# Optimization experiments

Measured on AMD Instinct MI355X. Metric: run time of the kernel, lower is better.

## Reference

```python
import jax, jax.numpy as jnp
import numpy as np

N = 3000          # num_sample (nodes)
N_OMICS = 3000    # input feature dims for both omics
ENC1, ENC2, NZ = 256, 128, 64


def _xavier(key, fan_in, fan_out):
    limit = float(np.sqrt(6.0 / (fan_in + fan_out)))
    return jax.random.uniform(key, (fan_in, fan_out), jnp.float32, -limit, limit)


def setup_inputs() -> dict:
    key = jax.random.key(0)
    ks = jax.random.split(key, 20)
    inp = {
        "omics_1": jax.random.normal(ks[0], (N, N_OMICS), jnp.float32),
        "omics_2": jax.random.normal(ks[1], (N, N_OMICS), jnp.float32),
    }
    # random dense adjacency, row-normalized (as a typical normalized graph operator)
    for i, name in enumerate(["adj_feature_omics1", "adj_feature_omics2",
                              "adj_spatial_omics1", "adj_spatial_omics2"]):
        a = jax.random.uniform(ks[2 + i], (N, N), jnp.float32)
        inp[name] = a / jnp.sum(a, axis=1, keepdims=True)
    # GNNLayer weights for the four GAE encoders (xavier uniform, as in reset_parameters)
    dims = [(N_OMICS, ENC1), (ENC1, ENC2), (ENC2, NZ)]
    kidx = 6
    for enc in ["f1", "f2", "s1", "s2"]:
        for li, (fi, fo) in enumerate(dims, start=1):
            inp[f"w_{enc}_{li}"] = _xavier(ks[kidx], fi, fo)
            kidx += 1
    return inp


def _gae_encoder(x, adj, w1, w2, w3):
    # GNNLayer: support = act(x @ W); out = spmm(adj, support). Dropout is identity (eval).
    z = adj @ jnp.tanh(x @ w1)          # [N, ENC1]
    z = adj @ jnp.tanh(z @ w2)          # [N, ENC2]
    z = adj @ (z @ w3)                  # [N, NZ]  (no activation on layer 3)
    adj_hat = jax.nn.sigmoid(z @ z.T)   # [N, N]
    return z, adj_hat


def reference(omics_1, omics_2,
              adj_feature_omics1, adj_feature_omics2,
              adj_spatial_omics1, adj_spatial_omics2,
              w_f1_1, w_f1_2, w_f1_3,
              w_f2_1, w_f2_2, w_f2_3,
              w_s1_1, w_s1_2, w_s1_3,
              w_s2_1, w_s2_2, w_s2_3):
    _, a1 = _gae_encoder(omics_1, adj_feature_omics1, w_f1_1, w_f1_2, w_f1_3)
    _, a2 = _gae_encoder(omics_2, adj_feature_omics2, w_f2_1, w_f2_2, w_f2_3)
    _, a3 = _gae_encoder(omics_1, adj_spatial_omics1, w_s1_1, w_s1_2, w_s1_3)
    _, a4 = _gae_encoder(omics_2, adj_spatial_omics2, w_s2_1, w_s2_2, w_s2_3)
    # stacked reconstructed adjacencies from the four encoders [4, N, N]
    return jnp.stack([a1, a2, a3, a4], axis=0)
```

## Files before the change

### kernel.cpp

```cpp
#include <hip/hip_runtime.h>
#include <stdint.h>
#include <stddef.h>


typedef __attribute__((ext_vector_type(8))) _Float16 half8;
typedef __attribute__((ext_vector_type(4))) float f32x4;

#define PAD 3072
#define MR  3000
#define ADJ_STRIDE ((size_t)PAD * PAD)

static __device__ __forceinline__ void async_cp16(const _Float16* g, _Float16* l) {
    __builtin_amdgcn_global_load_lds((const __attribute__((address_space(1))) void*)g,
                                     (__attribute__((address_space(3))) void*)l, 16, 0, 0);
}

struct Wt12 { const float* src[12]; _Float16* dst[12];
              int fi[12]; int fo[12]; int ldk[12]; int nr[12]; };

__global__ __launch_bounds__(256) void wt_cast12(Wt12 p) {
    const int z   = blockIdx.y;
    const int idx = blockIdx.x * 256 + threadIdx.x;
    const int ldk = p.ldk[z];
    if (idx >= p.nr[z] * ldk) return;
    const int r = idx / ldk;
    const int k = idx - r * ldk;
    float v = 0.f;
    if (r < p.fo[z] && k < p.fi[z]) v = p.src[z][(size_t)k * p.fo[z] + r];
    p.dst[z][(size_t)r * ldk + k] = (_Float16)v;
}

struct GArgs {
    const _Float16* Aall; size_t aStride;
    const _Float16* Ball; size_t bStride;
    const float* Bf0; const float* Bf1;
    void* Call; size_t cStride;
    int M, Ncols, Kp, lda, ldb, ldc, mBound, nBound;
};

template<int ACT, int OMODE, int S, int BSRC>
static __device__ __forceinline__
void gemm_body(const GArgs& ga, int bx, int by, int bz, _Float16* smem)
{
    _Float16* As = smem;
    _Float16* Bs = smem + 8192;

    const int z   = bz;
    const int e   = z / S;
    const int ksl = z - e * S;
    const int Kslice = ga.Kp / S;
    const int kbase  = ksl * Kslice;

    const _Float16* A = ga.Aall + (size_t)e * ga.aStride;
    const _Float16* B = ga.Ball + (size_t)e * ga.bStride;
    const float*    Bf = (e & 1) ? ga.Bf1 : ga.Bf0;

    const int tm = bx * 128;
    const int tn = by * 128;
    const int t    = threadIdx.x;
    const int lane = t & 63;
    const int w    = t >> 6;
    const int wm   = (w >> 1) * 64;
    const int wn   = (w & 1) * 64;
    const int lr   = lane & 15;
    const int lg   = lane >> 4;

    f32x4 acc[4][4];
    const f32x4 zero = {0.f, 0.f, 0.f, 0.f};
    #pragma unroll
    for (int i = 0; i < 4; ++i)
        #pragma unroll
        for (int j = 0; j < 4; ++j) acc[i][j] = zero;

    const int nkt = Kslice >> 6;
    for (int kt = 0; kt < nkt; ++kt) {
        const int k0 = kbase + (kt << 6);
        #pragma unroll
        for (int i = 0; i < 4; ++i) {
            const int c = t + i * 256;
            const int row = c >> 3, slot = c & 7;
            const int ss = slot ^ (row & 7);
            async_cp16(A + (size_t)(tm + row) * ga.lda + k0 + ss * 8, &As[c * 8]);
        }
        if (BSRC) {
            #pragma unroll
            for (int i = 0; i < 4; ++i) {
                const int c = t + i * 256;
                const int row = c >> 3, g = c & 7;
                const int grow = tn + row;
                const int gcol = k0 + g * 8;
                half8 h;
                if (grow < MR && gcol < MR) {
                    const float* bp = Bf + (size_t)grow * MR + gcol;
                    f32x4 v0 = *(const f32x4*)bp;
                    f32x4 v1 = *(const f32x4*)(bp + 4);
                    #pragma unroll
                    for (int j = 0; j < 4; ++j) { h[j] = (_Float16)v0[j]; h[4 + j] = (_Float16)v1[j]; }
                } else {
                    #pragma unroll
                    for (int j = 0; j < 8; ++j) h[j] = (_Float16)0.f;
                }
                *(half8*)&Bs[row * 64 + ((g ^ (row & 7)) << 3)] = h;
            }
        } else {
            #pragma unroll
            for (int i = 0; i < 4; ++i) {
                const int c = t + i * 256;
                const int row = c >> 3, slot = c & 7;
                const int ss = slot ^ (row & 7);
                async_cp16(B + (size_t)(tn + row) * ga.ldb + k0 + ss * 8, &Bs[c * 8]);
            }
        }
        __syncthreads();

        #pragma unroll
        for (int ks = 0; ks < 2; ++ks) {
            half8 af[4], bf[4];
            #pragma unroll
            for (int mi = 0; mi < 4; ++mi) {
                const int ra = wm + mi * 16 + lr;
                const int s  = (ks * 4 + lg) ^ (ra & 7);
                af[mi] = *(const half8*)((const char*)As + ra * 128 + s * 16);
            }
            #pragma unroll
            for (int ni = 0; ni < 4; ++ni) {
                const int rb = wn + ni * 16 + lr;
                const int s  = (ks * 4 + lg) ^ (rb & 7);
                bf[ni] = *(const half8*)((const char*)Bs + rb * 128 + s * 16);
            }
            #pragma unroll
            for (int mi = 0; mi < 4; ++mi)
                #pragma unroll
                for (int ni = 0; ni < 4; ++ni)
                    acc[mi][ni] = __builtin_amdgcn_mfma_f32_16x16x32_f16(
                        af[mi], bf[ni], acc[mi][ni], 0, 0, 0);
        }
        __syncthreads();
    }

    if (OMODE == 0) {
        _Float16* C = (_Float16*)ga.Call + (size_t)e * ga.cStride;
        #pragma unroll
        for (int mi = 0; mi < 4; ++mi)
            #pragma unroll
            for (int rr = 0; rr < 4; ++rr) {
                const int m = tm + wm + mi * 16 + lg * 4 + rr;
                #pragma unroll
                for (int ni = 0; ni < 4; ++ni) {
                    const int n = tn + wn + ni * 16 + lr;
                    float x = acc[mi][ni][rr];
                    if (ACT) x = tanhf(x);
                    const bool ok = (m < ga.M) && (n < ga.Ncols);
                    C[(size_t)m * ga.ldc + n] = ok ? (_Float16)x : (_Float16)0.f;
                }
            }
    } else {
        float* Cp = (float*)ga.Call + (size_t)(OMODE == 3 ? z : e) * ga.cStride;
        float* ep = (float*)smem + w * 2048;
        #pragma unroll
        for (int hs = 0; hs < 2; ++hs) {
            __syncthreads();
            #pragma unroll
            for (int mi2 = 0; mi2 < 2; ++mi2)
                #pragma unroll
                for (int ni = 0; ni < 4; ++ni)
                    #pragma unroll
                    for (int rr = 0; rr < 4; ++rr) {
                        const int row = mi2 * 16 + lg * 4 + rr;
                        const int col = ni * 16 + lr;
                        const int sw  = (((row ^ (row >> 2)) & 3) << 4);
                        ep[row * 64 + (col ^ sw)] = acc[hs * 2 + mi2][ni][rr];
                    }
            __syncthreads();
            #pragma unroll
            for (int r2 = 0; r2 < 8; ++r2) {
                const int row = r2 * 4 + (lane >> 4);
                const int c4  = (lane & 15) * 4;
                const int sw  = (((row ^ (row >> 2)) & 3) << 4);
                f32x4 v = *(const f32x4*)&ep[row * 64 + (c4 ^ sw)];
                const int gm = tm + wm + hs * 32 + row;
                const int gn = tn + wn + c4;
                if (gm < ga.mBound && gn < ga.nBound) {
                    if (OMODE == 2) {
                        #pragma unroll
                        for (int j = 0; j < 4; ++j)
                            v[j] = 1.0f / (1.0f + __expf(-v[j]));
                    }
                    *(f32x4*)&Cp[(size_t)gm * ga.ldc + gn] = v;
                }
            }
        }
    }
}

template<int ACT, int OMODE, int S, int BSRC>
__global__ __launch_bounds__(256, 2)
void gemm_bt(GArgs ga) {
    __shared__ _Float16 smem[16384];
    gemm_body<ACT, OMODE, S, BSRC>(ga, blockIdx.x, blockIdx.y, blockIdx.z, smem);
}

struct Adj4 { const float* src[4]; };

__global__ __launch_bounds__(256, 2)
void fused_s1(GArgs ga, Adj4 a4, _Float16* __restrict__ adst)
{
    __shared__ _Float16 smem[16384];
    const int b = blockIdx.x;
    if (b < 768) {
        const int bz = b & 15;
        const int r  = b >> 4;
        gemm_body<0, 3, 4, 1>(ga, r & 1, r >> 1, bz, smem);
    } else {
        const int cb  = b - 768;
        const int zz  = cb / 2304;
        const int idx = (cb - zz * 2304) * 256 + threadIdx.x;
        const int row = idx / 192;
        const int u   = idx - row * 192;
        const int c0  = u * 16;
        const float* sp = a4.src[zz] + (size_t)row * MR + c0;
        _Float16* d = adst + (size_t)zz * ADJ_STRIDE + (size_t)row * PAD + c0;
        half8 h0, h1;
        const bool rok = row < MR;
        if (rok && c0 < MR) {
            f32x4 v0 = __builtin_nontemporal_load((const f32x4*)sp);
            f32x4 v1 = __builtin_nontemporal_load((const f32x4*)(sp + 4));
            #pragma unroll
            for (int j = 0; j < 4; ++j) { h0[j] = (_Float16)v0[j]; h0[4 + j] = (_Float16)v1[j]; }
        } else {
            #pragma unroll
            for (int j = 0; j < 8; ++j) h0[j] = (_Float16)0.f;
        }
        if (rok && c0 + 8 < MR) {
            f32x4 v2 = __builtin_nontemporal_load((const f32x4*)(sp + 8));
            f32x4 v3 = __builtin_nontemporal_load((const f32x4*)(sp + 12));
            #pragma unroll
            for (int j = 0; j < 4; ++j) { h1[j] = (_Float16)v2[j]; h1[4 + j] = (_Float16)v3[j]; }
        } else {
            #pragma unroll
            for (int j = 0; j < 8; ++j) h1[j] = (_Float16)0.f;
        }
        *(half8*)d = h0;
        *(half8*)(d + 8) = h1;
    }
}

template<int ACT, int S>
__global__ __launch_bounds__(256)
void reduce_k(const float* __restrict__ P, _Float16* __restrict__ out, size_t region)
{
    const size_t e    = blockIdx.y;
    const size_t base = (size_t)(blockIdx.x * 256 + threadIdx.x) * 8;
    const float* p0 = P + e * S * region + base;
    f32x4 s0 = {0.f, 0.f, 0.f, 0.f}, s1 = s0;
    #pragma unroll
    for (int s = 0; s < S; ++s) {
        const float* p = p0 + (size_t)s * region;
        s0 += *(const f32x4*)p;
        s1 += *(const f32x4*)(p + 4);
    }
    half8 h;
    #pragma unroll
    for (int j = 0; j < 8; ++j) {
        float x = (j < 4) ? s0[j] : s1[j - 4];
        if (ACT) x = tanhf(x);
        h[j] = (_Float16)x;
    }
    *(half8*)(out + e * region + base) = h;
}

extern "C" void kernel_launch(void* const* d_in, const int* in_sizes, int n_in,
                              void* d_out, int out_size, void* d_ws, size_t ws_size,
                              hipStream_t stream)
{
    const float* X1 = (const float*)d_in[0];
    const float* X2 = (const float*)d_in[1];

    const size_t R1 = 786432;
    const size_t R2 = 393216;

    _Float16* Adj  = (_Float16*)d_out;
    float*    Part = (float*)(Adj + 4 * ADJ_STRIDE);

    _Float16* hb = (_Float16*)d_ws;
    size_t off = 0;
    auto alloc = [&](size_t elems) { _Float16* p = hb + off; off += elems; return p; };
    _Float16* T1  = alloc(4 * R1);
    _Float16* Z1  = alloc(4 * R1);
    _Float16* T2  = alloc(4 * R2);
    _Float16* Z2  = alloc(4 * R2);
    _Float16* T3  = alloc(4 * R2);
    _Float16* Z3  = alloc(4 * R2);
    _Float16* W1t = alloc(4ull * 256 * PAD);
    _Float16* W2t = alloc(4ull * 128 * 256);
    _Float16* W3t = alloc(4ull * 128 * 128);

    Wt12 w12;
    for (int enc = 0; enc < 4; ++enc) {
        w12.src[enc]     = (const float*)d_in[6 + enc * 3 + 0];
        w12.dst[enc]     = W1t + (size_t)enc * 256 * PAD;
        w12.fi[enc] = MR;  w12.fo[enc] = 256; w12.ldk[enc] = PAD; w12.nr[enc] = 256;

        w12.src[4 + enc] = (const float*)d_in[6 + enc * 3 + 1];
        w12.dst[4 + enc] = W2t + (size_t)enc * 128 * 256;
        w12.fi[4 + enc] = 256; w12.fo[4 + enc] = 128; w12.ldk[4 + enc] = 256; w12.nr[4 + enc] = 128;

        w12.src[8 + enc] = (const float*)d_in[6 + enc * 3 + 2];
        w12.dst[8 + enc] = W3t + (size_t)enc * 128 * 128;
        w12.fi[8 + enc] = 128; w12.fo[8 + enc] = 64; w12.ldk[8 + enc] = 128; w12.nr[8 + enc] = 128;
    }
    wt_cast12<<<dim3(3072, 12, 1), 256, 0, stream>>>(w12);

    const int BIG = 1 << 30;

    GArgs g1 = { W1t, (size_t)256 * PAD, nullptr, 0, X1, X2,
                 Part, R1, 256, PAD, PAD, PAD, MR, PAD, BIG, BIG };
    Adj4 a4;
    for (int i = 0; i < 4; ++i) a4.src[i] = (const float*)d_in[2 + i];
    fused_s1<<<dim3(9984, 1, 1), 256, 0, stream>>>(g1, a4, Adj);
    reduce_k<1, 4><<<dim3(384, 4, 1), 256, 0, stream>>>(Part, T1, R1);

    GArgs g2 = { Adj, ADJ_STRIDE, T1, R1, nullptr, nullptr,
                 Part, R1, PAD, 256, PAD, PAD, PAD, 256, BIG, BIG };
    gemm_bt<0, 3, 4, 0><<<dim3(24, 2, 16), 256, 0, stream>>>(g2);
    reduce_k<0, 4><<<dim3(384, 4, 1), 256, 0, stream>>>(Part, Z1, R1);

    GArgs g3 = { W2t, (size_t)128 * 256, Z1, R1, nullptr, nullptr,
                 Part, R2, 128, PAD, 256, 256, 256, PAD, BIG, BIG };
    gemm_bt<0, 3, 2, 0><<<dim3(1, 24, 8), 256, 0, stream>>>(g3);
    reduce_k<1, 2><<<dim3(192, 4, 1), 256, 0, stream>>>(Part, T2, R2);

    GArgs g4 = { Adj, ADJ_STRIDE, T2, R2, nullptr, nullptr,
                 Part, R2, PAD, 128, PAD, PAD, PAD, 128, BIG, BIG };
    gemm_bt<0, 3, 8, 0><<<dim3(24, 1, 32), 256, 0, stream>>>(g4);
    reduce_k<0, 8><<<dim3(192, 4, 1), 256, 0, stream>>>(Part, Z2, R2);

    GArgs g5 = { W3t, (size_t)128 * 128, Z2, R2, nullptr, nullptr,
                 T3, R2, 128, PAD, 128, 128, 128, PAD, BIG, BIG };
    gemm_bt<0, 0, 1, 0><<<dim3(1, 24, 4), 256, 0, stream>>>(g5);

    GArgs g6 = { Adj, ADJ_STRIDE, T3, R2, nullptr, nullptr,
                 Part, R2, PAD, 128, PAD, PAD, PAD, 128, BIG, BIG };
    gemm_bt<0, 3, 8, 0><<<dim3(24, 1, 32), 256, 0, stream>>>(g6);
    reduce_k<0, 8><<<dim3(192, 4, 1), 256, 0, stream>>>(Part, Z3, R2);

    GArgs g7 = { Z3, R2, Z3, R2, nullptr, nullptr,
                 d_out, (size_t)MR * MR, MR, MR, 64, 128, 128, MR, MR, MR };
    gemm_bt<0, 2, 1, 0><<<dim3(24, 24, 4), 256, 0, stream>>>(g7);
}
```

Measured before the change: 274.4 us.

## Pre-cast omics to fp16 and drop split-K for feature-projection GEMMs

Measured after the change: 282.2 us. 1.03x slower.

```diff
diff --git a/kernel.cpp b/kernel.cpp
--- a/kernel.cpp
+++ b/kernel.cpp
@@ -15,30 +15,94 @@
                                      (__attribute__((address_space(3))) void*)l, 16, 0, 0);
 }
 
-struct Wt12 { const float* src[12]; _Float16* dst[12];
-              int fi[12]; int fo[12]; int ldk[12]; int nr[12]; };
-
-__global__ __launch_bounds__(256) void wt_cast12(Wt12 p) {
-    const int z   = blockIdx.y;
-    const int idx = blockIdx.x * 256 + threadIdx.x;
-    const int ldk = p.ldk[z];
-    if (idx >= p.nr[z] * ldk) return;
-    const int r = idx / ldk;
-    const int k = idx - r * ldk;
-    float v = 0.f;
-    if (r < p.fo[z] && k < p.fi[z]) v = p.src[z][(size_t)k * p.fo[z] + r];
-    p.dst[z][(size_t)r * ldk + k] = (_Float16)v;
+struct PrepArgs {
+    const float* X[2]; _Float16* Xh;
+    const float* Wsrc[12];
+    _Float16* Wdst[3];
+};
+
+__global__ __launch_bounds__(256) void prep(PrepArgs p) {
+    __shared__ _Float16 lt[64 * 64];
+    const int b = blockIdx.x;
+    const int t = threadIdx.x;
+    if (b < 4608) {
+        const int which = b / 2304;
+        const int idx = (b - which * 2304) * 256 + t;
+        const int row = idx / 192;
+        const int c0  = (idx - row * 192) * 16;
+        const float* sp = p.X[which] + (size_t)row * MR + c0;
+        _Float16* d = p.Xh + (size_t)which * ADJ_STRIDE + (size_t)row * PAD + c0;
+        half8 h0, h1;
+        const bool rok = row < MR;
+        if (rok && c0 < MR) {
+            f32x4 v0 = __builtin_nontemporal_load((const f32x4*)sp);
+            f32x4 v1 = __builtin_nontemporal_load((const f32x4*)(sp + 4));
+            #pragma unroll
+            for (int j = 0; j < 4; ++j) { h0[j] = (_Float16)v0[j]; h0[4 + j] = (_Float16)v1[j]; }
+        } else {
+            #pragma unroll
+            for (int j = 0; j < 8; ++j) h0[j] = (_Float16)0.f;
+        }
+        if (rok && c0 + 8 < MR) {
+            f32x4 v2 = __builtin_nontemporal_load((const f32x4*)(sp + 8));
+            f32x4 v3 = __builtin_nontemporal_load((const f32x4*)(sp + 12));
+            #pragma unroll
+            for (int j = 0; j < 4; ++j) { h1[j] = (_Float16)v2[j]; h1[4 + j] = (_Float16)v3[j]; }
+        } else {
+            #pragma unroll
+            for (int j = 0; j < 8; ++j) h1[j] = (_Float16)0.f;
+        }
+        *(half8*)d = h0;
+        *(half8*)(d + 8) = h1;
+    } else {
+        const int b2  = b - 4608;
+        const int enc = b2 / 204;
+        int rem = b2 - enc * 204;
+        const float* src; _Float16* dst; int fi, fo, ldk, kt, rt;
+        if (rem < 192) {
+            src = p.Wsrc[enc * 3 + 0]; dst = p.Wdst[0] + (size_t)enc * 256 * PAD;
+            fi = MR; fo = 256; ldk = PAD; kt = rem >> 2; rt = rem & 3;
+        } else if (rem < 200) {
+            rem -= 192;
+            src = p.Wsrc[enc * 3 + 1]; dst = p.Wdst[1] + (size_t)enc * 128 * 256;
+            fi = 256; fo = 128; ldk = 256; kt = rem >> 1; rt = rem & 1;
+        } else {
+            rem -= 200;
+            src = p.Wsrc[enc * 3 + 2]; dst = p.Wdst[2] + (size_t)enc * 128 * 128;
+            fi = 128; fo = 64; ldk = 128; kt = rem >> 1; rt = rem & 1;
+        }
+        const int k0 = kt * 64, r0 = rt * 64;
+        {
+            const int kr = t >> 2, cc = (t & 3) << 4;
+            const int gk = k0 + kr;
+            const bool kok = gk < fi;
+            #pragma unroll
+            for (int j = 0; j < 16; ++j) {
+                const int gr = r0 + cc + j;
+                const float v = (kok && gr < fo) ? src[(size_t)gk * fo + gr] : 0.f;
+                lt[(cc + j) * 64 + kr] = (_Float16)v;
+            }
+        }
+        __syncthreads();
+        {
+            const int rr = t >> 2, kk = (t & 3) << 4;
+            half8 a  = *(half8*)&lt[rr * 64 + kk];
+            half8 bb = *(half8*)&lt[rr * 64 + kk + 8];
+            _Float16* dp = dst + (size_t)(r0 + rr) * ldk + k0 + kk;
+            *(half8*)dp = a;
+            *(half8*)(dp + 8) = bb;
+        }
+    }
 }
 
 struct GArgs {
-    const _Float16* Aall; size_t aStride;
-    const _Float16* Ball; size_t bStride;
-    const float* Bf0; const float* Bf1;
+    const _Float16* Aall; size_t aStride; int aMask;
+    const _Float16* Ball; size_t bStride; int bMask;
     void* Call; size_t cStride;
     int M, Ncols, Kp, lda, ldb, ldc, mBound, nBound;
 };
 
-template<int ACT, int OMODE, int S, int BSRC>
+template<int ACT, int OMODE, int S>
 static __device__ __forceinline__
 void gemm_body(const GArgs& ga, int bx, int by, int bz, _Float16* smem)
 {
@@ -51,9 +115,8 @@
     const int Kslice = ga.Kp / S;
     const int kbase  = ksl * Kslice;
 
-    const _Float16* A = ga.Aall + (size_t)e * ga.aStride;
-    const _Float16* B = ga.Ball + (size_t)e * ga.bStride;
-    const float*    Bf = (e & 1) ? ga.Bf1 : ga.Bf0;
+    const _Float16* A = ga.Aall + (size_t)(e & ga.aMask) * ga.aStride;
+    const _Float16* B = ga.Ball + (size_t)(e & ga.bMask) * ga.bStride;
 
     const int tm = bx * 128;
     const int tn = by * 128;
@@ -82,34 +145,12 @@
             const int ss = slot ^ (row & 7);
             async_cp16(A + (size_t)(tm + row) * ga.lda + k0 + ss * 8, &As[c * 8]);
         }
-        if (BSRC) {
-            #pragma unroll
-            for (int i = 0; i < 4; ++i) {
-                const int c = t + i * 256;
-                const int row = c >> 3, g = c & 7;
-                const int grow = tn + row;
-                const int gcol = k0 + g * 8;
-                half8 h;
-                if (grow < MR && gcol < MR) {
-                    const float* bp = Bf + (size_t)grow * MR + gcol;
-                    f32x4 v0 = *(const f32x4*)bp;
-                    f32x4 v1 = *(const f32x4*)(bp + 4);
-                    #pragma unroll
-                    for (int j = 0; j < 4; ++j) { h[j] = (_Float16)v0[j]; h[4 + j] = (_Float16)v1[j]; }
-                } else {
-                    #pragma unroll
-                    for (int j = 0; j < 8; ++j) h[j] = (_Float16)0.f;
-                }
-                *(half8*)&Bs[row * 64 + ((g ^ (row & 7)) << 3)] = h;
-            }
-        } else {
-            #pragma unroll
-            for (int i = 0; i < 4; ++i) {
-                const int c = t + i * 256;
-                const int row = c >> 3, slot = c & 7;
-                const int ss = slot ^ (row & 7);
-                async_cp16(B + (size_t)(tn + row) * ga.ldb + k0 + ss * 8, &Bs[c * 8]);
-            }
+        #pragma unroll
+        for (int i = 0; i < 4; ++i) {
+            const int c = t + i * 256;
+            const int row = c >> 3, slot = c & 7;
+            const int ss = slot ^ (row & 7);
+            async_cp16(B + (size_t)(tn + row) * ga.ldb + k0 + ss * 8, &Bs[c * 8]);
         }
         __syncthreads();
 
@@ -193,11 +234,11 @@
     }
 }
 
-template<int ACT, int OMODE, int S, int BSRC>
+template<int ACT, int OMODE, int S>
 __global__ __launch_bounds__(256, 2)
 void gemm_bt(GArgs ga) {
     __shared__ _Float16 smem[16384];
-    gemm_body<ACT, OMODE, S, BSRC>(ga, blockIdx.x, blockIdx.y, blockIdx.z, smem);
+    gemm_body<ACT, OMODE, S>(ga, blockIdx.x, blockIdx.y, blockIdx.z, smem);
 }
 
 struct Adj4 { const float* src[4]; };
@@ -207,12 +248,12 @@
 {
     __shared__ _Float16 smem[16384];
     const int b = blockIdx.x;
-    if (b < 768) {
-        const int bz = b & 15;
-        const int r  = b >> 4;
-        gemm_body<0, 3, 4, 1>(ga, r & 1, r >> 1, bz, smem);
+    if (b < 192) {
+        const int e   = b / 48;
+        const int rem = b - e * 48;
+        gemm_body<1, 0, 1>(ga, rem & 1, rem >> 1, e, smem);
     } else {
-        const int cb  = b - 768;
+        const int cb  = b - 192;
         const int zz  = cb / 2304;
         const int idx = (cb - zz * 2304) * 256 + threadIdx.x;
         const int row = idx / 192;
@@ -245,7 +286,7 @@
     }
 }
 
-template<int ACT, int S>
+template<int S>
 __global__ __launch_bounds__(256)
 void reduce_k(const float* __restrict__ P, _Float16* __restrict__ out, size_t region)
 {
@@ -261,11 +302,8 @@
     }
     half8 h;
     #pragma unroll
-    for (int j = 0; j < 8; ++j) {
-        float x = (j < 4) ? s0[j] : s1[j - 4];
-        if (ACT) x = tanhf(x);
-        h[j] = (_Float16)x;
-    }
+    for (int j = 0; j < 8; ++j)
+        h[j] = (_Float16)((j < 4) ? s0[j] : s1[j - 4]);
     *(half8*)(out + e * region + base) = h;
 }
 
@@ -273,9 +311,6 @@
                               void* d_out, int out_size, void* d_ws, size_t ws_size,
                               hipStream_t stream)
 {
-    const float* X1 = (const float*)d_in[0];
-    const float* X2 = (const float*)d_in[1];
-
     const size_t R1 = 786432;
     const size_t R2 = 393216;
 
@@ -285,6 +320,7 @@
     _Float16* hb = (_Float16*)d_ws;
     size_t off = 0;
     auto alloc = [&](size_t elems) { _Float16* p = hb + off; off += elems; return p; };
+    _Float16* Xh  = alloc(2 * ADJ_STRIDE);
     _Float16* T1  = alloc(4 * R1);
     _Float16* Z1  = alloc(4 * R1);
     _Float16* T2  = alloc(4 * R2);
@@ -295,56 +331,48 @@
     _Float16* W2t = alloc(4ull * 128 * 256);
     _Float16* W3t = alloc(4ull * 128 * 128);
 
-    Wt12 w12;
-    for (int enc = 0; enc < 4; ++enc) {
-        w12.src[enc]     = (const float*)d_in[6 + enc * 3 + 0];
-        w12.dst[enc]     = W1t + (size_t)enc * 256 * PAD;
-        w12.fi[enc] = MR;  w12.fo[enc] = 256; w12.ldk[enc] = PAD; w12.nr[enc] = 256;
-
-        w12.src[4 + enc] = (const float*)d_in[6 + enc * 3 + 1];
-        w12.dst[4 + enc] = W2t + (size_t)enc * 128 * 256;
-        w12.fi[4 + enc] = 256; w12.fo[4 + enc] = 128; w12.ldk[4 + enc] = 256; w12.nr[4 + enc] = 128;
-
-        w12.src[8 + enc] = (const float*)d_in[6 + enc * 3 + 2];
-        w12.dst[8 + enc] = W3t + (size_t)enc * 128 * 128;
-        w12.fi[8 + enc] = 128; w12.fo[8 + enc] = 64; w12.ldk[8 + enc] = 128; w12.nr[8 + enc] = 128;
-    }
-    wt_cast12<<<dim3(3072, 12, 1), 256, 0, stream>>>(w12);
+    PrepArgs pa;
+    pa.X[0] = (const float*)d_in[0];
+    pa.X[1] = (const float*)d_in[1];
+    pa.Xh = Xh;
+    for (int enc = 0; enc < 4; ++enc)
+        for (int li = 0; li < 3; ++li)
+            pa.Wsrc[enc * 3 + li] = (const float*)d_in[6 + enc * 3 + li];
+    pa.Wdst[0] = W1t; pa.Wdst[1] = W2t; pa.Wdst[2] = W3t;
+    prep<<<dim3(5424, 1, 1), 256, 0, stream>>>(pa);
 
     const int BIG = 1 << 30;
 
-    GArgs g1 = { W1t, (size_t)256 * PAD, nullptr, 0, X1, X2,
-                 Part, R1, 256, PAD, PAD, PAD, MR, PAD, BIG, BIG };
+    GArgs g1 = { W1t, (size_t)256 * PAD, 3, Xh, ADJ_STRIDE, 1,
+                 T1, R1, 256, PAD, PAD, PAD, PAD, PAD, BIG, BIG };
     Adj4 a4;
     for (int i = 0; i < 4; ++i) a4.src[i] = (const float*)d_in[2 + i];
-    fused_s1<<<dim3(9984, 1, 1), 256, 0, stream>>>(g1, a4, Adj);
-    reduce_k<1, 4><<<dim3(384, 4, 1), 256, 0, stream>>>(Part, T1, R1);
-
-    GArgs g2 = { Adj, ADJ_STRIDE, T1, R1, nullptr, nullptr,
+    fused_s1<<<dim3(9408, 1, 1), 256, 0, stream>>>(g1, a4, Adj);
+
+    GArgs g2 = { Adj, ADJ_STRIDE, 3, T1, R1, 3,
                  Part, R1, PAD, 256, PAD, PAD, PAD, 256, BIG, BIG };
-    gemm_bt<0, 3, 4, 0><<<dim3(24, 2, 16), 256, 0, stream>>>(g2);
-    reduce_k<0, 4><<<dim3(384, 4, 1), 256, 0, stream>>>(Part, Z1, R1);
-
-    GArgs g3 = { W2t, (size_t)128 * 256, Z1, R1, nullptr, nullptr,
-                 Part, R2, 128, PAD, 256, 256, 256, PAD, BIG, BIG };
-    gemm_bt<0, 3, 2, 0><<<dim3(1, 24, 8), 256, 0, stream>>>(g3);
-    reduce_k<1, 2><<<dim3(192, 4, 1), 256, 0, stream>>>(Part, T2, R2);
-
-    GArgs g4 = { Adj, ADJ_STRIDE, T2, R2, nullptr, nullptr,
+    gemm_bt<0, 3, 4><<<dim3(24, 2, 16), 256, 0, stream>>>(g2);
+    reduce_k<4><<<dim3(384, 4, 1), 256, 0, stream>>>(Part, Z1, R1);
+
+    GArgs g3 = { W2t, (size_t)128 * 256, 3, Z1, R1, 3,
+                 T2, R2, 128, PAD, 256, 256, 256, PAD, BIG, BIG };
+    gemm_bt<1, 0, 1><<<dim3(1, 24, 4), 256, 0, stream>>>(g3);
+
+    GArgs g4 = { Adj, ADJ_STRIDE, 3, T2, R2, 3,
                  Part, R2, PAD, 128, PAD, PAD, PAD, 128, BIG, BIG };
-    gemm_bt<0, 3, 8, 0><<<dim3(24, 1, 32), 256, 0, stream>>>(g4);
-    reduce_k<0, 8><<<dim3(192, 4, 1), 256, 0, stream>>>(Part, Z2, R2);
-
-    GArgs g5 = { W3t, (size_t)128 * 128, Z2, R2, nullptr, nullptr,
+    gemm_bt<0, 3, 8><<<dim3(24, 1, 32), 256, 0, stream>>>(g4);
+    reduce_k<8><<<dim3(192, 4, 1), 256, 0, stream>>>(Part, Z2, R2);
+
+    GArgs g5 = { W3t, (size_t)128 * 128, 3, Z2, R2, 3,
                  T3, R2, 128, PAD, 128, 128, 128, PAD, BIG, BIG };
-    gemm_bt<0, 0, 1, 0><<<dim3(1, 24, 4), 256, 0, stream>>>(g5);
-
-    GArgs g6 = { Adj, ADJ_STRIDE, T3, R2, nullptr, nullptr,
+    gemm_bt<0, 0, 1><<<dim3(1, 24, 4), 256, 0, stream>>>(g5);
+
+    GArgs g6 = { Adj, ADJ_STRIDE, 3, T3, R2, 3,
                  Part, R2, PAD, 128, PAD, PAD, PAD, 128, BIG, BIG };
-    gemm_bt<0, 3, 8, 0><<<dim3(24, 1, 32), 256, 0, stream>>>(g6);
-    reduce_k<0, 8><<<dim3(192, 4, 1), 256, 0, stream>>>(Part, Z3, R2);
-
-    GArgs g7 = { Z3, R2, Z3, R2, nullptr, nullptr,
+    gemm_bt<0, 3, 8><<<dim3(24, 1, 32), 256, 0, stream>>>(g6);
+    reduce_k<8><<<dim3(192, 4, 1), 256, 0, stream>>>(Part, Z3, R2);
+
+    GArgs g7 = { Z3, R2, 3, Z3, R2, 3,
                  d_out, (size_t)MR * MR, MR, MR, 64, 128, 128, MR, MR, MR };
-    gemm_bt<0, 2, 1, 0><<<dim3(24, 24, 4), 256, 0, stream>>>(g7);
-}
+    gemm_bt<0, 2, 1><<<dim3(24, 24, 4), 256, 0, stream>>>(g7);
+}
```
